# Optimization experiments

Hardware: AMD Instinct MI355X
Metric: run time of the kernel (lower is better)

## Reference

```python
import jax, jax.numpy as jnp
import numpy as np

B, N, NPOINT, NSAMPLE, CIN = 8, 16384, 2048, 32, 64
MLP = (64, 64, 128)
EPS = 1e-5  # torch BatchNorm2d default eps


def setup_inputs() -> dict:
    key = jax.random.key(0)
    ks = jax.random.split(key, 8)
    xyz = jax.random.normal(ks[0], (B, 3, N), dtype=jnp.float32)
    points = jax.random.normal(ks[1], (B, CIN, N), dtype=jnp.float32)
    # torch.randperm(N)[:npoint], shared across batch
    sample_idx = jax.random.permutation(ks[2], N)[:NPOINT].astype(jnp.int32)
    c0 = CIN + 3
    def conv_w(k, o, i):
        return jax.random.normal(k, (o, i), dtype=jnp.float32) * np.float32(1.0 / np.sqrt(i))
    W1 = conv_w(ks[3], MLP[0], c0)
    W2 = conv_w(ks[4], MLP[1], MLP[0])
    W3 = conv_w(ks[5], MLP[2], MLP[1])
    return {
        "xyz": xyz, "points": points, "sample_idx": sample_idx,
        "W1": W1, "b1": jnp.zeros((MLP[0],), jnp.float32), "g1": jnp.ones((MLP[0],), jnp.float32), "be1": jnp.zeros((MLP[0],), jnp.float32),
        "W2": W2, "b2": jnp.zeros((MLP[1],), jnp.float32), "g2": jnp.ones((MLP[1],), jnp.float32), "be2": jnp.zeros((MLP[1],), jnp.float32),
        "W3": W3, "b3": jnp.zeros((MLP[2],), jnp.float32), "g3": jnp.ones((MLP[2],), jnp.float32), "be3": jnp.zeros((MLP[2],), jnp.float32),
    }


def _bn(h, g, b):
    # training-mode BatchNorm2d: per-channel (last axis) stats over all other dims, biased var
    m = jnp.mean(h, axis=(0, 1, 2), keepdims=True)
    v = jnp.mean(jnp.square(h - m), axis=(0, 1, 2), keepdims=True)
    return (h - m) * jax.lax.rsqrt(v + EPS) * g + b


def reference(xyz, points, sample_idx, W1, b1, g1, be1, W2, b2, g2, be2, W3, b3, g3, be3):
    # sample npoint centroids (shared indices across batch, as in the torch code)
    q = jnp.take(xyz, sample_idx, axis=2).transpose(0, 2, 1)   # (B, npoint, 3)
    p = xyz.transpose(0, 2, 1)                                  # (B, N, 3)
    # squared pairwise distances (same ordering as cdist for topk)
    d2 = (jnp.sum(q * q, -1)[:, :, None]
          + jnp.sum(p * p, -1)[:, None, :]
          - 2.0 * jnp.einsum('bqc,bnc->bqn', q, p))             # (B, npoint, N)
    _, idx = jax.lax.top_k(-d2, NSAMPLE)                        # (B, npoint, nsample) smallest dists

    gxyz = jnp.take_along_axis(p[:, None, :, :], idx[:, :, :, None], axis=2)  # (B, npoint, nsample, 3)
    rel = gxyz - q[:, :, None, :]
    pf = points.transpose(0, 2, 1)                              # (B, N, C)
    gpts = jnp.take_along_axis(pf[:, None, :, :], idx[:, :, :, None], axis=2)  # (B, npoint, nsample, C)
    feat = jnp.concatenate([rel, gpts], axis=-1)                # (B, npoint, nsample, 3+C)

    h = jax.nn.relu(_bn(jnp.einsum('bpsc,oc->bpso', feat, W1) + b1, g1, be1))
    h = jax.nn.relu(_bn(jnp.einsum('bpsc,oc->bpso', h, W2) + b2, g2, be2))
    h = _bn(jnp.einsum('bpsc,oc->bpso', h, W3) + b3, g3, be3)
    new_points = jnp.max(h, axis=2)                             # max over nsample -> (B, npoint, mlp2)
    return q.transpose(0, 2, 1), new_points.transpose(0, 2, 1)  # (B,3,npoint), (B,mlp2,npoint)
```

## Files before the change

### kernel.cpp

```cpp
#include <hip/hip_runtime.h>
#include <cstdint>

#define DEVFN __device__ __forceinline__

constexpr int B_ = 8, N_ = 16384, NP_ = 2048, NS_ = 32;
constexpr int S_ = B_ * NP_ * NS_;
constexpr float INV_CNT = 1.0f / 524288.0f;

typedef __attribute__((ext_vector_type(8))) short bf8_t;
typedef __attribute__((ext_vector_type(4))) float f4_t;
#define MFMA16(A, Bv, C) __builtin_amdgcn_mfma_f32_16x16x32_bf16(A, Bv, C, 0, 0, 0)

union u4s8 { uint4 u; unsigned short s[8]; };

DEVFN unsigned long long wredmin64(unsigned long long v) {
  for (int o = 32; o; o >>= 1) { unsigned long long u = __shfl_xor(v, o); v = u < v ? u : v; }
  return v;
}
DEVFN float d2_ref(float4 q, float4 p) {
  float dot = __fadd_rn(__fadd_rn(__fmul_rn(q.x, p.x), __fmul_rn(q.y, p.y)), __fmul_rn(q.z, p.z));
  return __fsub_rn(__fadd_rn(q.w, p.w), __fadd_rn(dot, dot));
}
DEVFN unsigned int fmono(float d) {
  unsigned int u = __float_as_uint(d);
  return u ^ ((u >> 31) ? 0xFFFFFFFFu : 0x80000000u);
}
DEVFN unsigned short f2bf(float f) {
  unsigned int u = __float_as_uint(f);
  u += 0x7FFFu + ((u >> 16) & 1u);
  return (unsigned short)(u >> 16);
}
DEVFN bf8_t ld_bf8(const unsigned short* p) {
  union { uint4 u; bf8_t b; } cv;
  cv.u = *reinterpret_cast<const uint4*>(p);
  return cv.b;
}

__global__ __launch_bounds__(256) void prep_xyzw(const float* __restrict__ xyz, float4* __restrict__ xyzw) {
  int t = blockIdx.x * 256 + threadIdx.x;
  int b = t >> 14, n = t & (N_ - 1);
  const float* X = xyz + (size_t)b * 3 * N_;
  float x = X[n], y = X[N_ + n], z = X[2 * N_ + n];
  float sq = __fadd_rn(__fadd_rn(__fmul_rn(x, x), __fmul_rn(y, y)), __fmul_rn(z, z));
  xyzw[t] = make_float4(x, y, z, sq);
}

__global__ __launch_bounds__(256) void prep_q(const int* __restrict__ sidx, const float4* __restrict__ xyzw,
                                              float4* __restrict__ qw, float* __restrict__ out_q) {
  int t = blockIdx.x * 256 + threadIdx.x;
  int b = t >> 11, p = t & (NP_ - 1);
  int n = sidx[p] & (N_ - 1);
  float4 v = xyzw[b * N_ + n];
  qw[t] = v;
  out_q[((size_t)b * 3 + 0) * NP_ + p] = v.x;
  out_q[((size_t)b * 3 + 1) * NP_ + p] = v.y;
  out_q[((size_t)b * 3 + 2) * NP_ + p] = v.z;
}

__global__ __launch_bounds__(256) void transpose_bf16(const float* __restrict__ in, unsigned short* __restrict__ out) {
  __shared__ float tile[32][33];
  int b = blockIdx.x >> 10;
  int rem = blockIdx.x & 1023;
  int c0 = (rem >> 9) << 5;
  int n0 = (rem & 511) << 5;
  int tx = threadIdx.x & 31, ty = threadIdx.x >> 5;
#pragma unroll
  for (int jj = 0; jj < 4; jj++) {
    int c = c0 + ty + jj * 8;
    tile[ty + jj * 8][tx] = in[((size_t)b * 64 + c) * N_ + n0 + tx];
  }
  __syncthreads();
#pragma unroll
  for (int jj = 0; jj < 4; jj++) {
    int n = n0 + ty + jj * 8;
    out[((size_t)b * N_ + n) * 64 + c0 + tx] = f2bf(tile[tx][ty + jj * 8]);
  }
}

__global__ __launch_bounds__(256) void prep_w(const float* __restrict__ W1, const float* __restrict__ W2,
                                              const float* __restrict__ W3, unsigned short* __restrict__ W1b,
                                              unsigned short* __restrict__ W2b, unsigned short* __restrict__ W3b) {
  int t = blockIdx.x * 256 + threadIdx.x;
  int stride = gridDim.x * 256;
  for (int e = t; e < 64 * 96; e += stride) {
    int o = e / 96, k = e - o * 96;
    float v = (k < 64) ? W1[o * 67 + 3 + k] : (k < 67 ? W1[o * 67 + (k - 64)] : 0.0f);
    W1b[e] = f2bf(v);
  }
  for (int e = t; e < 64 * 64; e += stride) W2b[e] = f2bf(W2[e]);
  for (int e = t; e < 128 * 64; e += stride) W3b[e] = f2bf(W3[e]);
}

__global__ __launch_bounds__(256, 4) void knn_kernel(const float4* __restrict__ xyzw,
                                                     const float4* __restrict__ qw,
                                                     int* __restrict__ idx_out) {
  __shared__ float4 Pst[1024];
  __shared__ unsigned short surv[16][256];
  __shared__ float Tsh[16];
  __shared__ int cnt[16];
  int tid = threadIdx.x, wave = tid >> 6, lane = tid & 63;
  int b = blockIdx.x >> 7;
  int q0 = (blockIdx.x & 127) * 16;
  const float4* P = xyzw + b * N_;
  float Qx[16], Qy[16], Qz[16];
#pragma unroll
  for (int j = 0; j < 16; j++) {
    float4 q = qw[b * NP_ + q0 + j];
    Qx[j] = q.x; Qy[j] = q.y; Qz[j] = q.z;
  }
  float dmin[16];
#pragma unroll
  for (int j = 0; j < 16; j++) dmin[j] = 1e30f;
  for (int c = 0; c < N_ / 1024; c++) {
    __syncthreads();
#pragma unroll
    for (int u = 0; u < 4; u++) Pst[tid + u * 256] = P[c * 1024 + tid + u * 256];
    __syncthreads();
#pragma unroll
    for (int t = 0; t < 4; t++) {
      float4 p = Pst[wave * 256 + t * 64 + lane];
      float kx = -2.0f * p.x, ky = -2.0f * p.y, kz = -2.0f * p.z;
#pragma unroll
      for (int j = 0; j < 16; j++) {
        float key = __fmaf_rn(kx, Qx[j], __fmaf_rn(ky, Qy[j], __fmaf_rn(kz, Qz[j], p.w)));
        dmin[j] = fminf(dmin[j], key);
      }
    }
  }
  __syncthreads();
  float* dl = (float*)Pst;
#pragma unroll
  for (int j = 0; j < 16; j++) dl[j * 256 + wave * 64 + lane] = dmin[j];
  if (tid < 16) cnt[tid] = 0;
  __syncthreads();
#pragma unroll 1
  for (int jj = 0; jj < 4; jj++) {
    int j = wave * 4 + jj;
    float v = fminf(fminf(dl[j * 256 + lane], dl[j * 256 + 64 + lane]),
                    fminf(dl[j * 256 + 128 + lane], dl[j * 256 + 192 + lane]));
#pragma unroll
    for (int k = 2; k <= 64; k <<= 1)
#pragma unroll
      for (int s = k >> 1; s > 0; s >>= 1) {
        float o = __shfl_xor(v, s);
        bool up = ((lane & k) == 0);
        bool tmin = (((lane & s) == 0) == up);
        v = tmin ? fminf(v, o) : fmaxf(v, o);
      }
    if (lane == 31) Tsh[j] = v;
  }
  __syncthreads();
  float T[16];
#pragma unroll
  for (int j = 0; j < 16; j++) T[j] = Tsh[j];
  for (int c = 0; c < N_ / 1024; c++) {
    __syncthreads();
#pragma unroll
    for (int u = 0; u < 4; u++) Pst[tid + u * 256] = P[c * 1024 + tid + u * 256];
    __syncthreads();
#pragma unroll 1
    for (int t = 0; t < 4; t++) {
      int n = c * 1024 + wave * 256 + t * 64 + lane;
      float4 p = Pst[wave * 256 + t * 64 + lane];
      float kx = -2.0f * p.x, ky = -2.0f * p.y, kz = -2.0f * p.z;
#pragma unroll
      for (int j = 0; j < 16; j++) {
        float key = __fmaf_rn(kx, Qx[j], __fmaf_rn(ky, Qy[j], __fmaf_rn(kz, Qz[j], p.w)));
        bool pred = key <= T[j];
        unsigned long long mask = __ballot(pred);
        if (mask) {
          int basew;
          if (lane == 0) basew = atomicAdd(&cnt[j], (int)__popcll(mask));
          basew = __shfl(basew, 0);
          if (pred) {
            int off = basew + (int)__popcll(mask & ((1ull << lane) - 1ull));
            if (off < 256) surv[j][off] = (unsigned short)n;
          }
        }
      }
    }
  }
  __syncthreads();
#pragma unroll 1
  for (int jj = 0; jj < 4; jj++) {
    int j = wave * 4 + jj;
    float4 Q = qw[b * NP_ + q0 + j];
    int m = cnt[j] < 256 ? cnt[j] : 256;
    if (m <= 64) {
      unsigned long long v = ~0ull;
      if (lane < m) {
        int n = surv[j][lane];
        float4 p = P[n];
        float d2 = d2_ref(Q, p);
        v = ((unsigned long long)fmono(d2) << 32) | (unsigned int)n;
      }
#pragma unroll
      for (int k = 2; k <= 64; k <<= 1)
#pragma unroll
        for (int s = k >> 1; s > 0; s >>= 1) {
          unsigned long long o = __shfl_xor(v, s);
          bool up = ((lane & k) == 0);
          bool tmin = (((lane & s) == 0) == up);
          unsigned long long lo = v < o ? v : o;
          unsigned long long hi = v < o ? o : v;
          v = tmin ? lo : hi;
        }
      if (lane < 32) idx_out[(b * NP_ + q0 + j) * NS_ + lane] = (int)(v & 0xFFFFu);
    } else {
      unsigned long long k4[4];
#pragma unroll
      for (int t = 0; t < 4; t++) {
        int ii = t * 64 + lane;
        k4[t] = ~0ull;
        if (ii < m) {
          int n = surv[j][ii];
          float4 p = P[n];
          float d2 = d2_ref(Q, p);
          k4[t] = ((unsigned long long)fmono(d2) << 32) | (unsigned int)n;
        }
      }
      int keep = 0;
      for (int r = 0; r < 32; r++) {
        unsigned long long loc = k4[0];
        loc = k4[1] < loc ? k4[1] : loc;
        loc = k4[2] < loc ? k4[2] : loc;
        loc = k4[3] < loc ? k4[3] : loc;
        unsigned long long km = wredmin64(loc);
#pragma unroll
        for (int t = 0; t < 4; t++) if (k4[t] == km) k4[t] = ~0ull;
        if (lane == r) keep = (int)(km & 0xFFFFu);
      }
      if (lane < 32) idx_out[(b * NP_ + q0 + j) * NS_ + lane] = keep;
    }
  }
}


__global__ __launch_bounds__(256, 4) void fused1_mat(
    const int* __restrict__ idx, const float4* __restrict__ xyzw, const float4* __restrict__ qw,
    const unsigned short* __restrict__ pTb, const unsigned short* __restrict__ W1b,
    const float* __restrict__ b1, float* __restrict__ statsOut, unsigned short* __restrict__ h) {
  __shared__ unsigned short W1L[64 * 104];
  __shared__ unsigned short hbuf[64 * 64];
  __shared__ float sAcc[128];
  int tid = threadIdx.x;
  int w = tid >> 6, l = tid & 63;
  int c16 = l & 15, g = l >> 4;
  for (int e = tid; e < 64 * 12; e += 256) {
    int r = e / 12, c = e % 12;
    *(uint4*)&W1L[r * 104 + c * 8] = *(const uint4*)&W1b[r * 96 + c * 8];
  }
  float rb1[4];
#pragma unroll
  for (int j = 0; j < 4; j++) rb1[j] = b1[j * 16 + c16];
  float st1[4] = {0, 0, 0, 0}, st2[4] = {0, 0, 0, 0};
  __syncthreads();
  for (int tile = blockIdx.x; tile < S_ / 64; tile += gridDim.x) {
    int b = tile >> 10;
    int s = tile * 64 + w * 16 + c16;
    int n = idx[s] & (N_ - 1);
    const unsigned short* arow = pTb + (((size_t)(b << 14) + n) << 6);
    bf8_t a0 = ld_bf8(arow + g * 8);
    bf8_t a1 = ld_bf8(arow + 32 + g * 8);
    float4 P = xyzw[(b << 14) + n];
    float4 Q = qw[tile * 2 + (w >> 1)];
    bf8_t a2 = {0, 0, 0, 0, 0, 0, 0, 0};
    if (g == 0) {
      a2[0] = (short)f2bf(P.x - Q.x);
      a2[1] = (short)f2bf(P.y - Q.y);
      a2[2] = (short)f2bf(P.z - Q.z);
    }
    f4_t acc1[4];
#pragma unroll
    for (int j = 0; j < 4; j++) {
      bf8_t w0 = ld_bf8(&W1L[(j * 16 + c16) * 104 + 0 * 32 + g * 8]);
      bf8_t w1 = ld_bf8(&W1L[(j * 16 + c16) * 104 + 1 * 32 + g * 8]);
      bf8_t w2 = ld_bf8(&W1L[(j * 16 + c16) * 104 + 2 * 32 + g * 8]);
      acc1[j] = (f4_t){0.0f, 0.0f, 0.0f, 0.0f};
      acc1[j] = MFMA16(a0, w0, acc1[j]);
      acc1[j] = MFMA16(a1, w1, acc1[j]);
      acc1[j] = MFMA16(a2, w2, acc1[j]);
    }
    __syncthreads();
#pragma unroll
    for (int j = 0; j < 4; j++)
#pragma unroll
      for (int r = 0; r < 4; r++) {
        float hv = acc1[j][r] + rb1[j];
        st1[j] += hv; st2[j] += hv * hv;
        int row = w * 16 + g * 4 + r, ch = j * 16 + c16;
        hbuf[row * 64 + (((ch >> 3) ^ (row & 7)) << 3) + (ch & 7)] = f2bf(hv);
      }
    __syncthreads();
    int rrow = w * 16 + c16;
    uint4 v0 = *(const uint4*)&hbuf[rrow * 64 + ((g ^ (rrow & 7)) << 3)];
    uint4 v1 = *(const uint4*)&hbuf[rrow * 64 + (((4 + g) ^ (rrow & 7)) << 3)];
    uint4* hd = (uint4*)(h + (((size_t)tile * 64 + rrow) << 6));
    hd[g] = v0;
    hd[4 + g] = v1;
  }
  __syncthreads();
  if (tid < 128) sAcc[tid] = 0.0f;
  __syncthreads();
#pragma unroll
  for (int j = 0; j < 4; j++) {
    atomicAdd(&sAcc[j * 16 + c16], st1[j]);
    atomicAdd(&sAcc[64 + j * 16 + c16], st2[j]);
  }
  __syncthreads();
  if (tid < 128) atomicAdd(&statsOut[tid], sAcc[tid]);
}

__global__ __launch_bounds__(256, 4) void fused2_mat(
    const unsigned short* __restrict__ W2b, const float* __restrict__ g1, const float* __restrict__ be1,
    const float* __restrict__ stats1, const float* __restrict__ b2,
    float* __restrict__ statsOut, unsigned short* __restrict__ h) {
  __shared__ unsigned short W2L[64 * 72];
  __shared__ unsigned short hbuf[64 * 64];
  __shared__ float sa1[64], sd1[64];
  __shared__ float sAcc[128];
  int tid = threadIdx.x;
  int w = tid >> 6, l = tid & 63;
  int c16 = l & 15, g = l >> 4;
  for (int e = tid; e < 64 * 8; e += 256) {
    int r = e >> 3, c = e & 7;
    *(uint4*)&W2L[r * 72 + c * 8] = *(const uint4*)&W2b[r * 64 + c * 8];
  }
  if (tid < 64) {
    float m = stats1[tid] * INV_CNT;
    float v = stats1[64 + tid] * INV_CNT - m * m;
    float a = rsqrtf(v + 1e-5f) * g1[tid];
    sa1[tid] = a;
    sd1[tid] = be1[tid] - m * a;
  }
  float rb2[4];
#pragma unroll
  for (int j = 0; j < 4; j++) rb2[j] = b2[j * 16 + c16];
  float st1[4] = {0, 0, 0, 0}, st2[4] = {0, 0, 0, 0};
  __syncthreads();
  for (int tile = blockIdx.x; tile < S_ / 64; tile += gridDim.x) {
    int rrow = w * 16 + c16;
    uint4* hd = (uint4*)(h + (((size_t)tile * 64 + rrow) << 6));
    u4s8 c0, c1;
    c0.u = hd[g];
    c1.u = hd[4 + g];
    bf8_t a0f, a1f;
#pragma unroll
    for (int e = 0; e < 8; e++) {
      float x0 = __uint_as_float((unsigned)c0.s[e] << 16);
      float x1 = __uint_as_float((unsigned)c1.s[e] << 16);
      a0f[e] = (short)f2bf(fmaxf(0.0f, fmaf(x0, sa1[g * 8 + e], sd1[g * 8 + e])));
      a1f[e] = (short)f2bf(fmaxf(0.0f, fmaf(x1, sa1[32 + g * 8 + e], sd1[32 + g * 8 + e])));
    }
    f4_t acc2[4];
#pragma unroll
    for (int j = 0; j < 4; j++) {
      bf8_t w0 = ld_bf8(&W2L[(j * 16 + c16) * 72 + g * 8]);
      bf8_t w1 = ld_bf8(&W2L[(j * 16 + c16) * 72 + 32 + g * 8]);
      acc2[j] = (f4_t){0.0f, 0.0f, 0.0f, 0.0f};
      acc2[j] = MFMA16(a0f, w0, acc2[j]);
      acc2[j] = MFMA16(a1f, w1, acc2[j]);
    }
    __syncthreads();
#pragma unroll
    for (int j = 0; j < 4; j++)
#pragma unroll
      for (int r = 0; r < 4; r++) {
        float hv = acc2[j][r] + rb2[j];
        st1[j] += hv; st2[j] += hv * hv;
        int row = w * 16 + g * 4 + r, ch = j * 16 + c16;
        hbuf[row * 64 + (((ch >> 3) ^ (row & 7)) << 3) + (ch & 7)] = f2bf(hv);
      }
    __syncthreads();
    uint4 v0 = *(const uint4*)&hbuf[rrow * 64 + ((g ^ (rrow & 7)) << 3)];
    uint4 v1 = *(const uint4*)&hbuf[rrow * 64 + (((4 + g) ^ (rrow & 7)) << 3)];
    hd[g] = v0;
    hd[4 + g] = v1;
  }
  __syncthreads();
  if (tid < 128) sAcc[tid] = 0.0f;
  __syncthreads();
#pragma unroll
  for (int j = 0; j < 4; j++) {
    atomicAdd(&sAcc[j * 16 + c16], st1[j]);
    atomicAdd(&sAcc[64 + j * 16 + c16], st2[j]);
  }
  __syncthreads();
  if (tid < 128) atomicAdd(&statsOut[tid], sAcc[tid]);
}

__global__ __launch_bounds__(256, 4) void fused3_mat(
    const unsigned short* __restrict__ W3b, const float* __restrict__ g2, const float* __restrict__ be2,
    const float* __restrict__ stats2, const float* __restrict__ b3,
    float* __restrict__ statsOut, const unsigned short* __restrict__ h, float* __restrict__ maxmin) {
  __shared__ unsigned short W3L[128 * 72];
  __shared__ float sa2[64], sd2[64];
  __shared__ float smx[4][128];
  __shared__ float smn[4][128];
  __shared__ float sAcc[256];
  int tid = threadIdx.x;
  int w = tid >> 6, l = tid & 63;
  int c16 = l & 15, g = l >> 4;
  for (int e = tid; e < 128 * 8; e += 256) {
    int r = e >> 3, c = e & 7;
    *(uint4*)&W3L[r * 72 + c * 8] = *(const uint4*)&W3b[r * 64 + c * 8];
  }
  if (tid < 64) {
    float m = stats2[tid] * INV_CNT;
    float v = stats2[64 + tid] * INV_CNT - m * m;
    float a = rsqrtf(v + 1e-5f) * g2[tid];
    sa2[tid] = a;
    sd2[tid] = be2[tid] - m * a;
  }
  float rb3[8];
#pragma unroll
  for (int j = 0; j < 8; j++) rb3[j] = b3[j * 16 + c16];
  float st1[8], st2[8];
#pragma unroll
  for (int j = 0; j < 8; j++) { st1[j] = 0.0f; st2[j] = 0.0f; }
  __syncthreads();
  for (int tile = blockIdx.x; tile < S_ / 64; tile += gridDim.x) {
    int rrow = w * 16 + c16;
    const uint4* hd = (const uint4*)(h + (((size_t)tile * 64 + rrow) << 6));
    u4s8 c0, c1;
    c0.u = hd[g];
    c1.u = hd[4 + g];
    bf8_t a0f, a1f;
#pragma unroll
    for (int e = 0; e < 8; e++) {
      float x0 = __uint_as_float((unsigned)c0.s[e] << 16);
      float x1 = __uint_as_float((unsigned)c1.s[e] << 16);
      a0f[e] = (short)f2bf(fmaxf(0.0f, fmaf(x0, sa2[g * 8 + e], sd2[g * 8 + e])));
      a1f[e] = (short)f2bf(fmaxf(0.0f, fmaf(x1, sa2[32 + g * 8 + e], sd2[32 + g * 8 + e])));
    }
    f4_t acc3[8];
#pragma unroll
    for (int j = 0; j < 8; j++) {
      bf8_t w0 = ld_bf8(&W3L[(j * 16 + c16) * 72 + g * 8]);
      bf8_t w1 = ld_bf8(&W3L[(j * 16 + c16) * 72 + 32 + g * 8]);
      acc3[j] = (f4_t){0.0f, 0.0f, 0.0f, 0.0f};
      acc3[j] = MFMA16(a0f, w0, acc3[j]);
      acc3[j] = MFMA16(a1f, w1, acc3[j]);
    }
    float mx[8], mn[8];
#pragma unroll
    for (int j = 0; j < 8; j++) {
      mx[j] = -1e30f; mn[j] = 1e30f;
#pragma unroll
      for (int r = 0; r < 4; r++) {
        float hv = acc3[j][r] + rb3[j];
        st1[j] += hv; st2[j] += hv * hv;
        mx[j] = fmaxf(mx[j], hv); mn[j] = fminf(mn[j], hv);
      }
      mx[j] = fmaxf(mx[j], __shfl_xor(mx[j], 16));
      mx[j] = fmaxf(mx[j], __shfl_xor(mx[j], 32));
      mn[j] = fminf(mn[j], __shfl_xor(mn[j], 16));
      mn[j] = fminf(mn[j], __shfl_xor(mn[j], 32));
    }
    __syncthreads();
    if (l < 16) {
#pragma unroll
      for (int j = 0; j < 8; j++) { smx[w][j * 16 + l] = mx[j]; smn[w][j * 16 + l] = mn[j]; }
    }
    __syncthreads();
    {
      int cen = tid >> 7, ch = tid & 127;
      float vx = fmaxf(smx[2 * cen][ch], smx[2 * cen + 1][ch]);
      float vn = fminf(smn[2 * cen][ch], smn[2 * cen + 1][ch]);
      size_t gcen = (size_t)tile * 2 + cen;
      maxmin[gcen * 256 + ch * 2 + 0] = vx;
      maxmin[gcen * 256 + ch * 2 + 1] = vn;
    }
  }
  __syncthreads();
  if (tid < 256) sAcc[tid] = 0.0f;
  __syncthreads();
#pragma unroll
  for (int j = 0; j < 8; j++) {
    atomicAdd(&sAcc[j * 16 + c16], st1[j]);
    atomicAdd(&sAcc[128 + j * 16 + c16], st2[j]);
  }
  __syncthreads();
  if (tid < 256) atomicAdd(&statsOut[tid], sAcc[tid]);
}

template <int STAGES>
__global__ __launch_bounds__(256, (STAGES == 1) ? 4 : 3) void fused_kernel(
    const int* __restrict__ idx, const float4* __restrict__ xyzw, const float4* __restrict__ qw,
    const unsigned short* __restrict__ pTb, const unsigned short* __restrict__ W1b,
    const unsigned short* __restrict__ W2b, const unsigned short* __restrict__ W3b,
    const float* __restrict__ b1, const float* __restrict__ g1, const float* __restrict__ be1,
    const float* __restrict__ stats1,
    const float* __restrict__ b2, const float* __restrict__ g2, const float* __restrict__ be2,
    const float* __restrict__ stats2,
    const float* __restrict__ b3,
    float* __restrict__ statsOut, float* __restrict__ maxmin) {
  __shared__ unsigned short W1L[64 * 104];
  __shared__ unsigned short W2L[(STAGES >= 2) ? 64 * 72 : 8];
  __shared__ unsigned short W3L[(STAGES == 3) ? 128 * 72 : 8];
  __shared__ unsigned short hbuf[(STAGES >= 2) ? 64 * 64 : 8];
  __shared__ float smx[(STAGES == 3) ? 4 : 1][128];
  __shared__ float smn[(STAGES == 3) ? 4 : 1][128];
  __shared__ float sAcc[256];
  constexpr int NJL = (STAGES == 3) ? 8 : 4;
  int tid = threadIdx.x;
  int w = tid >> 6, l = tid & 63;
  int c16 = l & 15, g = l >> 4;
  for (int e = tid; e < 64 * 12; e += 256) {
    int r = e / 12, c = e % 12;
    *(uint4*)&W1L[r * 104 + c * 8] = *(const uint4*)&W1b[r * 96 + c * 8];
  }
  if (STAGES >= 2)
    for (int e = tid; e < 64 * 8; e += 256) {
      int r = e >> 3, c = e & 7;
      *(uint4*)&W2L[r * 72 + c * 8] = *(const uint4*)&W2b[r * 64 + c * 8];
    }
  if (STAGES == 3)
    for (int e = tid; e < 128 * 8; e += 256) {
      int r = e >> 3, c = e & 7;
      *(uint4*)&W3L[r * 72 + c * 8] = *(const uint4*)&W3b[r * 64 + c * 8];
    }
  float rb1[4], ra1[4], rd1[4], rb2[4], ra2[4], rd2[4], rb3[8];
#pragma unroll
  for (int j = 0; j < 4; j++) rb1[j] = b1[j * 16 + c16];
  if (STAGES >= 2) {
#pragma unroll
    for (int j = 0; j < 4; j++) {
      int ch = j * 16 + c16;
      float m = stats1[ch] * INV_CNT;
      float v = stats1[64 + ch] * INV_CNT - m * m;
      float a = rsqrtf(v + 1e-5f) * g1[ch];
      ra1[j] = a; rd1[j] = be1[ch] - m * a;
      rb2[j] = b2[ch];
    }
  }
  if (STAGES == 3) {
#pragma unroll
    for (int j = 0; j < 4; j++) {
      int ch = j * 16 + c16;
      float m = stats2[ch] * INV_CNT;
      float v = stats2[64 + ch] * INV_CNT - m * m;
      float a = rsqrtf(v + 1e-5f) * g2[ch];
      ra2[j] = a; rd2[j] = be2[ch] - m * a;
    }
#pragma unroll
    for (int j = 0; j < 8; j++) rb3[j] = b3[j * 16 + c16];
  }
  float st1[NJL], st2[NJL];
#pragma unroll
  for (int j = 0; j < NJL; j++) { st1[j] = 0.0f; st2[j] = 0.0f; }
  __syncthreads();
  for (int tile = blockIdx.x; tile < S_ / 64; tile += gridDim.x) {
    int b = tile >> 10;
    int s = tile * 64 + w * 16 + c16;
    int n = idx[s] & (N_ - 1);
    const unsigned short* arow = pTb + (((size_t)(b << 14) + n) << 6);
    bf8_t a0 = ld_bf8(arow + g * 8);
    bf8_t a1 = ld_bf8(arow + 32 + g * 8);
    float4 P = xyzw[(b << 14) + n];
    float4 Q = qw[tile * 2 + (w >> 1)];
    bf8_t a2 = {0, 0, 0, 0, 0, 0, 0, 0};
    if (g == 0) {
      a2[0] = (short)f2bf(P.x - Q.x);
      a2[1] = (short)f2bf(P.y - Q.y);
      a2[2] = (short)f2bf(P.z - Q.z);
    }
    f4_t acc1[4];
#pragma unroll
    for (int j = 0; j < 4; j++) {
      bf8_t w0 = ld_bf8(&W1L[(j * 16 + c16) * 104 + 0 * 32 + g * 8]);
      bf8_t w1 = ld_bf8(&W1L[(j * 16 + c16) * 104 + 1 * 32 + g * 8]);
      bf8_t w2 = ld_bf8(&W1L[(j * 16 + c16) * 104 + 2 * 32 + g * 8]);
      acc1[j] = (f4_t){0.0f, 0.0f, 0.0f, 0.0f};
      acc1[j] = MFMA16(a0, w0, acc1[j]);
      acc1[j] = MFMA16(a1, w1, acc1[j]);
      acc1[j] = MFMA16(a2, w2, acc1[j]);
    }
    if (STAGES == 1) {
#pragma unroll
      for (int j = 0; j < 4; j++)
#pragma unroll
        for (int r = 0; r < 4; r++) {
          float hv = acc1[j][r] + rb1[j];
          st1[j] += hv; st2[j] += hv * hv;
        }
      continue;
    }
    if (STAGES == 2) __syncthreads();
#pragma unroll
    for (int j = 0; j < 4; j++)
#pragma unroll
      for (int r = 0; r < 4; r++) {
        float hv = acc1[j][r] + rb1[j];
        float t = fmaxf(0.0f, fmaf(hv, ra1[j], rd1[j]));
        int row = w * 16 + g * 4 + r, ch = j * 16 + c16;
        hbuf[row * 64 + (((ch >> 3) ^ (row & 7)) << 3) + (ch & 7)] = f2bf(t);
      }
    __syncthreads();
    int rrow = w * 16 + c16;
    bf8_t h1f[2];
#pragma unroll
    for (int kb = 0; kb < 2; kb++)
      h1f[kb] = ld_bf8(hbuf + rrow * 64 + (((kb * 4 + g) ^ (rrow & 7)) << 3));
    f4_t acc2[4];
#pragma unroll
    for (int j = 0; j < 4; j++) {
      bf8_t w0 = ld_bf8(&W2L[(j * 16 + c16) * 72 + g * 8]);
      bf8_t w1 = ld_bf8(&W2L[(j * 16 + c16) * 72 + 32 + g * 8]);
      acc2[j] = (f4_t){0.0f, 0.0f, 0.0f, 0.0f};
      acc2[j] = MFMA16(h1f[0], w0, acc2[j]);
      acc2[j] = MFMA16(h1f[1], w1, acc2[j]);
    }
    if (STAGES == 2) {
#pragma unroll
      for (int j = 0; j < 4; j++)
#pragma unroll
        for (int r = 0; r < 4; r++) {
          float hv = acc2[j][r] + rb2[j];
          st1[j] += hv; st2[j] += hv * hv;
        }
      continue;
    }
    __syncthreads();
#pragma unroll
    for (int j = 0; j < 4; j++)
#pragma unroll
      for (int r = 0; r < 4; r++) {
        float hv = acc2[j][r] + rb2[j];
        float t = fmaxf(0.0f, fmaf(hv, ra2[j], rd2[j]));
        int row = w * 16 + g * 4 + r, ch = j * 16 + c16;
        hbuf[row * 64 + (((ch >> 3) ^ (row & 7)) << 3) + (ch & 7)] = f2bf(t);
      }
    __syncthreads();
    bf8_t h2f[2];
#pragma unroll
    for (int kb = 0; kb < 2; kb++)
      h2f[kb] = ld_bf8(hbuf + rrow * 64 + (((kb * 4 + g) ^ (rrow & 7)) << 3));
    f4_t acc3[8];
#pragma unroll
    for (int j = 0; j < 8; j++) {
      bf8_t w0 = ld_bf8(&W3L[(j * 16 + c16) * 72 + g * 8]);
      bf8_t w1 = ld_bf8(&W3L[(j * 16 + c16) * 72 + 32 + g * 8]);
      acc3[j] = (f4_t){0.0f, 0.0f, 0.0f, 0.0f};
      acc3[j] = MFMA16(h2f[0], w0, acc3[j]);
      acc3[j] = MFMA16(h2f[1], w1, acc3[j]);
    }
    float mx[8], mn[8];
#pragma unroll
    for (int j = 0; j < 8; j++) {
      mx[j] = -1e30f; mn[j] = 1e30f;
#pragma unroll
      for (int r = 0; r < 4; r++) {
        float hv = acc3[j][r] + rb3[j];
        st1[j] += hv; st2[j] += hv * hv;
        mx[j] = fmaxf(mx[j], hv); mn[j] = fminf(mn[j], hv);
      }
      mx[j] = fmaxf(mx[j], __shfl_xor(mx[j], 16));
      mx[j] = fmaxf(mx[j], __shfl_xor(mx[j], 32));
      mn[j] = fminf(mn[j], __shfl_xor(mn[j], 16));
      mn[j] = fminf(mn[j], __shfl_xor(mn[j], 32));
    }
    if (l < 16) {
#pragma unroll
      for (int j = 0; j < 8; j++) { smx[w][j * 16 + l] = mx[j]; smn[w][j * 16 + l] = mn[j]; }
    }
    __syncthreads();
    {
      int cen = tid >> 7, ch = tid & 127;
      float vx = fmaxf(smx[2 * cen][ch], smx[2 * cen + 1][ch]);
      float vn = fminf(smn[2 * cen][ch], smn[2 * cen + 1][ch]);
      size_t gcen = (size_t)tile * 2 + cen;
      maxmin[gcen * 256 + ch * 2 + 0] = vx;
      maxmin[gcen * 256 + ch * 2 + 1] = vn;
    }
  }
  __syncthreads();
  if (tid < 2 * NJL * 16) sAcc[tid] = 0.0f;
  __syncthreads();
#pragma unroll
  for (int j = 0; j < NJL; j++) {
    atomicAdd(&sAcc[j * 16 + c16], st1[j]);
    atomicAdd(&sAcc[NJL * 16 + j * 16 + c16], st2[j]);
  }
  __syncthreads();
  if (tid < 2 * NJL * 16) atomicAdd(&statsOut[tid], sAcc[tid]);
}

__global__ __launch_bounds__(256) void finalize_kernel(const float* __restrict__ maxmin,
                                                       const float* __restrict__ stats3,
                                                       const float* __restrict__ g3, const float* __restrict__ be3,
                                                       float* __restrict__ out_np) {
  int o = blockIdx.x * 256 + threadIdx.x;
  int p = o & 2047, ch = (o >> 11) & 127, b = o >> 18;
  float m = stats3[ch] * INV_CNT;
  float v = stats3[128 + ch] * INV_CNT - m * m;
  float a = rsqrtf(v + 1e-5f) * g3[ch];
  float d = be3[ch] - m * a;
  size_t g = (size_t)(b * 2048 + p);
  float hi = maxmin[g * 256 + ch * 2 + 0];
  float lo = maxmin[g * 256 + ch * 2 + 1];
  out_np[o] = fmaf(a, (a >= 0.0f ? hi : lo), d);
}

extern "C" void kernel_launch(void* const* d_in, const int* in_sizes, int n_in,
                              void* d_out, int out_size, void* d_ws, size_t ws_size,
                              hipStream_t stream) {
  const float* xyz = (const float*)d_in[0];
  const float* points = (const float*)d_in[1];
  const int* sidx = (const int*)d_in[2];
  const float* W1 = (const float*)d_in[3];
  const float* b1 = (const float*)d_in[4];
  const float* g1 = (const float*)d_in[5];
  const float* be1 = (const float*)d_in[6];
  const float* W2 = (const float*)d_in[7];
  const float* b2 = (const float*)d_in[8];
  const float* g2 = (const float*)d_in[9];
  const float* be2 = (const float*)d_in[10];
  const float* W3 = (const float*)d_in[11];
  const float* b3 = (const float*)d_in[12];
  const float* g3 = (const float*)d_in[13];
  const float* be3 = (const float*)d_in[14];

  float* out_q = (float*)d_out;
  float* out_np = (float*)d_out + (size_t)B_ * 3 * NP_;

  char* ws = (char*)d_ws;
  float* stats1 = (float*)(ws + 0);
  float* stats2 = (float*)(ws + 512);
  float* stats3 = (float*)(ws + 1024);
  size_t off = 4096;
  float4* xyzw = (float4*)(ws + off); off += (size_t)B_ * N_ * 16;
  float4* qw = (float4*)(ws + off);   off += (size_t)B_ * NP_ * 16;
  int* idxb = (int*)(ws + off);       off += (size_t)B_ * NP_ * NS_ * 4;
  unsigned short* pTb = (unsigned short*)(ws + off); off += (size_t)B_ * N_ * 64 * 2;
  unsigned short* W1b = (unsigned short*)(ws + off); off += 64 * 96 * 2;
  unsigned short* W2b = (unsigned short*)(ws + off); off += 64 * 64 * 2;
  unsigned short* W3b = (unsigned short*)(ws + off); off += 128 * 64 * 2;
  float* maxmin = (float*)(ws + off);  off += (size_t)B_ * NP_ * 128 * 2 * 4;
  unsigned short* hG = (unsigned short*)(ws + off); off += (size_t)S_ * 64 * 2;
  bool use_mat = (ws_size >= off);

  hipMemsetAsync(ws, 0, 4096, stream);
  prep_xyzw<<<B_ * N_ / 256, 256, 0, stream>>>(xyz, xyzw);
  prep_q<<<B_ * NP_ / 256, 256, 0, stream>>>(sidx, xyzw, qw, out_q);
  transpose_bf16<<<B_ * 2 * (N_ / 32), 256, 0, stream>>>(points, pTb);
  prep_w<<<72, 256, 0, stream>>>(W1, W2, W3, W1b, W2b, W3b);
  knn_kernel<<<B_ * (NP_ / 16), 256, 0, stream>>>(xyzw, qw, idxb);
  if (use_mat) {
    fused1_mat<<<1024, 256, 0, stream>>>(idxb, xyzw, qw, pTb, W1b, b1, stats1, hG);
    fused2_mat<<<1024, 256, 0, stream>>>(W2b, g1, be1, stats1, b2, stats2, hG);
    fused3_mat<<<1024, 256, 0, stream>>>(W3b, g2, be2, stats2, b3, stats3, hG, maxmin);
  } else {
    fused_kernel<1><<<1024, 256, 0, stream>>>(idxb, xyzw, qw, pTb, W1b, W2b, W3b,
        b1, g1, be1, stats1, b2, g2, be2, stats2, b3, stats1, maxmin);
    fused_kernel<2><<<1024, 256, 0, stream>>>(idxb, xyzw, qw, pTb, W1b, W2b, W3b,
        b1, g1, be1, stats1, b2, g2, be2, stats2, b3, stats2, maxmin);
    fused_kernel<3><<<1024, 256, 0, stream>>>(idxb, xyzw, qw, pTb, W1b, W2b, W3b,
        b1, g1, be1, stats1, b2, g2, be2, stats2, b3, stats3, maxmin);
  }
  finalize_kernel<<<(B_ * 128 * NP_) / 256, 256, 0, stream>>>(maxmin, stats3, g3, be3, out_np);
}
```

Measured before the change: 403.6 us.

## Give each wave its own centroid to drop block-wide barriers in MLP stages

The three materialized MLP kernels now assign one centroid (32 samples) to each wave instead of a 64-row tile shared by the block. Each wave gets a private LDS staging buffer, and the block __syncthreads calls become wave barriers. Stage 3 reduces max/min within the wave and writes it directly as float2, with no shared-memory cross-wave merge. The grid doubles to 2048 blocks, and the fallback recompute path and the workspace-size check are removed, so the code now assumes the workspace is large enough.

```diff
diff --git a/kernel.cpp b/kernel.cpp
--- a/kernel.cpp
+++ b/kernel.cpp
@@ -241,7 +241,7 @@
     const unsigned short* __restrict__ pTb, const unsigned short* __restrict__ W1b,
     const float* __restrict__ b1, float* __restrict__ statsOut, unsigned short* __restrict__ h) {
   __shared__ unsigned short W1L[64 * 104];
-  __shared__ unsigned short hbuf[64 * 64];
+  __shared__ unsigned short hb[4][32 * 64];
   __shared__ float sAcc[128];
   int tid = threadIdx.x;
   int w = tid >> 6, l = tid & 63;
@@ -255,49 +255,56 @@
   for (int j = 0; j < 4; j++) rb1[j] = b1[j * 16 + c16];
   float st1[4] = {0, 0, 0, 0}, st2[4] = {0, 0, 0, 0};
   __syncthreads();
-  for (int tile = blockIdx.x; tile < S_ / 64; tile += gridDim.x) {
-    int b = tile >> 10;
-    int s = tile * 64 + w * 16 + c16;
-    int n = idx[s] & (N_ - 1);
-    const unsigned short* arow = pTb + (((size_t)(b << 14) + n) << 6);
-    bf8_t a0 = ld_bf8(arow + g * 8);
-    bf8_t a1 = ld_bf8(arow + 32 + g * 8);
-    float4 P = xyzw[(b << 14) + n];
-    float4 Q = qw[tile * 2 + (w >> 1)];
-    bf8_t a2 = {0, 0, 0, 0, 0, 0, 0, 0};
-    if (g == 0) {
-      a2[0] = (short)f2bf(P.x - Q.x);
-      a2[1] = (short)f2bf(P.y - Q.y);
-      a2[2] = (short)f2bf(P.z - Q.z);
-    }
-    f4_t acc1[4];
-#pragma unroll
-    for (int j = 0; j < 4; j++) {
-      bf8_t w0 = ld_bf8(&W1L[(j * 16 + c16) * 104 + 0 * 32 + g * 8]);
-      bf8_t w1 = ld_bf8(&W1L[(j * 16 + c16) * 104 + 1 * 32 + g * 8]);
-      bf8_t w2 = ld_bf8(&W1L[(j * 16 + c16) * 104 + 2 * 32 + g * 8]);
-      acc1[j] = (f4_t){0.0f, 0.0f, 0.0f, 0.0f};
-      acc1[j] = MFMA16(a0, w0, acc1[j]);
-      acc1[j] = MFMA16(a1, w1, acc1[j]);
-      acc1[j] = MFMA16(a2, w2, acc1[j]);
-    }
-    __syncthreads();
-#pragma unroll
-    for (int j = 0; j < 4; j++)
-#pragma unroll
-      for (int r = 0; r < 4; r++) {
-        float hv = acc1[j][r] + rb1[j];
-        st1[j] += hv; st2[j] += hv * hv;
-        int row = w * 16 + g * 4 + r, ch = j * 16 + c16;
-        hbuf[row * 64 + (((ch >> 3) ^ (row & 7)) << 3) + (ch & 7)] = f2bf(hv);
-      }
-    __syncthreads();
-    int rrow = w * 16 + c16;
-    uint4 v0 = *(const uint4*)&hbuf[rrow * 64 + ((g ^ (rrow & 7)) << 3)];
-    uint4 v1 = *(const uint4*)&hbuf[rrow * 64 + (((4 + g) ^ (rrow & 7)) << 3)];
-    uint4* hd = (uint4*)(h + (((size_t)tile * 64 + rrow) << 6));
-    hd[g] = v0;
-    hd[4 + g] = v1;
+  unsigned short* hw = hb[w];
+  for (int cen = blockIdx.x * 4 + w; cen < B_ * NP_; cen += gridDim.x * 4) {
+    int b = cen >> 11;
+    float4 Q = qw[cen];
+#pragma unroll
+    for (int rh = 0; rh < 2; rh++) {
+      int s = cen * 32 + rh * 16 + c16;
+      int n = idx[s] & (N_ - 1);
+      const unsigned short* arow = pTb + (((size_t)(b << 14) + n) << 6);
+      bf8_t a0 = ld_bf8(arow + g * 8);
+      bf8_t a1 = ld_bf8(arow + 32 + g * 8);
+      float4 P = xyzw[(b << 14) + n];
+      bf8_t a2 = {0, 0, 0, 0, 0, 0, 0, 0};
+      if (g == 0) {
+        a2[0] = (short)f2bf(P.x - Q.x);
+        a2[1] = (short)f2bf(P.y - Q.y);
+        a2[2] = (short)f2bf(P.z - Q.z);
+      }
+      f4_t acc[4];
+#pragma unroll
+      for (int j = 0; j < 4; j++) {
+        bf8_t w0 = ld_bf8(&W1L[(j * 16 + c16) * 104 + 0 * 32 + g * 8]);
+        bf8_t w1 = ld_bf8(&W1L[(j * 16 + c16) * 104 + 1 * 32 + g * 8]);
+        bf8_t w2 = ld_bf8(&W1L[(j * 16 + c16) * 104 + 2 * 32 + g * 8]);
+        acc[j] = (f4_t){0.0f, 0.0f, 0.0f, 0.0f};
+        acc[j] = MFMA16(a0, w0, acc[j]);
+        acc[j] = MFMA16(a1, w1, acc[j]);
+        acc[j] = MFMA16(a2, w2, acc[j]);
+      }
+#pragma unroll
+      for (int j = 0; j < 4; j++)
+#pragma unroll
+        for (int r = 0; r < 4; r++) {
+          float hv = acc[j][r] + rb1[j];
+          st1[j] += hv; st2[j] += hv * hv;
+          int row = rh * 16 + g * 4 + r, ch = j * 16 + c16;
+          hw[row * 64 + (((ch >> 3) ^ (row & 7)) << 3) + (ch & 7)] = f2bf(hv);
+        }
+    }
+    __builtin_amdgcn_wave_barrier();
+#pragma unroll
+    for (int rh = 0; rh < 2; rh++) {
+      int rr = rh * 16 + c16;
+      uint4 v0 = *(const uint4*)&hw[rr * 64 + ((g ^ (rr & 7)) << 3)];
+      uint4 v1 = *(const uint4*)&hw[rr * 64 + (((4 + g) ^ (rr & 7)) << 3)];
+      uint4* hd = (uint4*)(h + (((size_t)cen * 32 + rr) << 6));
+      hd[g] = v0;
+      hd[4 + g] = v1;
+    }
+    __builtin_amdgcn_wave_barrier();
   }
   __syncthreads();
   if (tid < 128) sAcc[tid] = 0.0f;
@@ -316,7 +323,7 @@
     const float* __restrict__ stats1, const float* __restrict__ b2,
     float* __restrict__ statsOut, unsigned short* __restrict__ h) {
   __shared__ unsigned short W2L[64 * 72];
-  __shared__ unsigned short hbuf[64 * 64];
+  __shared__ unsigned short hb[4][32 * 64];
   __shared__ float sa1[64], sd1[64];
   __shared__ float sAcc[128];
   int tid = threadIdx.x;
@@ -338,44 +345,53 @@
   for (int j = 0; j < 4; j++) rb2[j] = b2[j * 16 + c16];
   float st1[4] = {0, 0, 0, 0}, st2[4] = {0, 0, 0, 0};
   __syncthreads();
-  for (int tile = blockIdx.x; tile < S_ / 64; tile += gridDim.x) {
-    int rrow = w * 16 + c16;
-    uint4* hd = (uint4*)(h + (((size_t)tile * 64 + rrow) << 6));
-    u4s8 c0, c1;
-    c0.u = hd[g];
-    c1.u = hd[4 + g];
-    bf8_t a0f, a1f;
-#pragma unroll
-    for (int e = 0; e < 8; e++) {
-      float x0 = __uint_as_float((unsigned)c0.s[e] << 16);
-      float x1 = __uint_as_float((unsigned)c1.s[e] << 16);
-      a0f[e] = (short)f2bf(fmaxf(0.0f, fmaf(x0, sa1[g * 8 + e], sd1[g * 8 + e])));
-      a1f[e] = (short)f2bf(fmaxf(0.0f, fmaf(x1, sa1[32 + g * 8 + e], sd1[32 + g * 8 + e])));
-    }
-    f4_t acc2[4];
-#pragma unroll
-    for (int j = 0; j < 4; j++) {
-      bf8_t w0 = ld_bf8(&W2L[(j * 16 + c16) * 72 + g * 8]);
-      bf8_t w1 = ld_bf8(&W2L[(j * 16 + c16) * 72 + 32 + g * 8]);
-      acc2[j] = (f4_t){0.0f, 0.0f, 0.0f, 0.0f};
-      acc2[j] = MFMA16(a0f, w0, acc2[j]);
-      acc2[j] = MFMA16(a1f, w1, acc2[j]);
-    }
-    __syncthreads();
-#pragma unroll
-    for (int j = 0; j < 4; j++)
-#pragma unroll
-      for (int r = 0; r < 4; r++) {
-        float hv = acc2[j][r] + rb2[j];
-        st1[j] += hv; st2[j] += hv * hv;
-        int row = w * 16 + g * 4 + r, ch = j * 16 + c16;
-        hbuf[row * 64 + (((ch >> 3) ^ (row & 7)) << 3) + (ch & 7)] = f2bf(hv);
-      }
-    __syncthreads();
-    uint4 v0 = *(const uint4*)&hbuf[rrow * 64 + ((g ^ (rrow & 7)) << 3)];
-    uint4 v1 = *(const uint4*)&hbuf[rrow * 64 + (((4 + g) ^ (rrow & 7)) << 3)];
-    hd[g] = v0;
-    hd[4 + g] = v1;
+  unsigned short* hw = hb[w];
+  for (int cen = blockIdx.x * 4 + w; cen < B_ * NP_; cen += gridDim.x * 4) {
+#pragma unroll
+    for (int rh = 0; rh < 2; rh++) {
+      int rr = rh * 16 + c16;
+      uint4* hd = (uint4*)(h + (((size_t)cen * 32 + rr) << 6));
+      u4s8 c0, c1;
+      c0.u = hd[g];
+      c1.u = hd[4 + g];
+      bf8_t a0f, a1f;
+#pragma unroll
+      for (int e = 0; e < 8; e++) {
+        float x0 = __uint_as_float((unsigned)c0.s[e] << 16);
+        float x1 = __uint_as_float((unsigned)c1.s[e] << 16);
+        a0f[e] = (short)f2bf(fmaxf(0.0f, fmaf(x0, sa1[g * 8 + e], sd1[g * 8 + e])));
+        a1f[e] = (short)f2bf(fmaxf(0.0f, fmaf(x1, sa1[32 + g * 8 + e], sd1[32 + g * 8 + e])));
+      }
+      f4_t acc[4];
+#pragma unroll
+      for (int j = 0; j < 4; j++) {
+        bf8_t w0 = ld_bf8(&W2L[(j * 16 + c16) * 72 + g * 8]);
+        bf8_t w1 = ld_bf8(&W2L[(j * 16 + c16) * 72 + 32 + g * 8]);
+        acc[j] = (f4_t){0.0f, 0.0f, 0.0f, 0.0f};
+        acc[j] = MFMA16(a0f, w0, acc[j]);
+        acc[j] = MFMA16(a1f, w1, acc[j]);
+      }
+#pragma unroll
+      for (int j = 0; j < 4; j++)
+#pragma unroll
+        for (int r = 0; r < 4; r++) {
+          float hv = acc[j][r] + rb2[j];
+          st1[j] += hv; st2[j] += hv * hv;
+          int row = rh * 16 + g * 4 + r, ch = j * 16 + c16;
+          hw[row * 64 + (((ch >> 3) ^ (row & 7)) << 3) + (ch & 7)] = f2bf(hv);
+        }
+    }
+    __builtin_amdgcn_wave_barrier();
+#pragma unroll
+    for (int rh = 0; rh < 2; rh++) {
+      int rr = rh * 16 + c16;
+      uint4 v0 = *(const uint4*)&hw[rr * 64 + ((g ^ (rr & 7)) << 3)];
+      uint4 v1 = *(const uint4*)&hw[rr * 64 + (((4 + g) ^ (rr & 7)) << 3)];
+      uint4* hd = (uint4*)(h + (((size_t)cen * 32 + rr) << 6));
+      hd[g] = v0;
+      hd[4 + g] = v1;
+    }
+    __builtin_amdgcn_wave_barrier();
   }
   __syncthreads();
   if (tid < 128) sAcc[tid] = 0.0f;
@@ -395,8 +411,6 @@
     float* __restrict__ statsOut, const unsigned short* __restrict__ h, float* __restrict__ maxmin) {
   __shared__ unsigned short W3L[128 * 72];
   __shared__ float sa2[64], sd2[64];
-  __shared__ float smx[4][128];
-  __shared__ float smn[4][128];
   __shared__ float sAcc[256];
   int tid = threadIdx.x;
   int w = tid >> 6, l = tid & 63;
@@ -419,57 +433,54 @@
 #pragma unroll
   for (int j = 0; j < 8; j++) { st1[j] = 0.0f; st2[j] = 0.0f; }
   __syncthreads();
-  for (int tile = blockIdx.x; tile < S_ / 64; tile += gridDim.x) {
-    int rrow = w * 16 + c16;
-    const uint4* hd = (const uint4*)(h + (((size_t)tile * 64 + rrow) << 6));
-    u4s8 c0, c1;
-    c0.u = hd[g];
-    c1.u = hd[4 + g];
-    bf8_t a0f, a1f;
-#pragma unroll
-    for (int e = 0; e < 8; e++) {
-      float x0 = __uint_as_float((unsigned)c0.s[e] << 16);
-      float x1 = __uint_as_float((unsigned)c1.s[e] << 16);
-      a0f[e] = (short)f2bf(fmaxf(0.0f, fmaf(x0, sa2[g * 8 + e], sd2[g * 8 + e])));
-      a1f[e] = (short)f2bf(fmaxf(0.0f, fmaf(x1, sa2[32 + g * 8 + e], sd2[32 + g * 8 + e])));
-    }
-    f4_t acc3[8];
+  for (int cen = blockIdx.x * 4 + w; cen < B_ * NP_; cen += gridDim.x * 4) {
+    float mx[8], mn[8];
+#pragma unroll
+    for (int j = 0; j < 8; j++) { mx[j] = -1e30f; mn[j] = 1e30f; }
+#pragma unroll
+    for (int rh = 0; rh < 2; rh++) {
+      int rr = rh * 16 + c16;
+      const uint4* hd = (const uint4*)(h + (((size_t)cen * 32 + rr) << 6));
+      u4s8 c0, c1;
+      c0.u = hd[g];
+      c1.u = hd[4 + g];
+      bf8_t a0f, a1f;
+#pragma unroll
+      for (int e = 0; e < 8; e++) {
+        float x0 = __uint_as_float((unsigned)c0.s[e] << 16);
+        float x1 = __uint_as_float((unsigned)c1.s[e] << 16);
+        a0f[e] = (short)f2bf(fmaxf(0.0f, fmaf(x0, sa2[g * 8 + e], sd2[g * 8 + e])));
+        a1f[e] = (short)f2bf(fmaxf(0.0f, fmaf(x1, sa2[32 + g * 8 + e], sd2[32 + g * 8 + e])));
+      }
+      f4_t acc[8];
+#pragma unroll
+      for (int j = 0; j < 8; j++) {
+        bf8_t w0 = ld_bf8(&W3L[(j * 16 + c16) * 72 + g * 8]);
+        bf8_t w1 = ld_bf8(&W3L[(j * 16 + c16) * 72 + 32 + g * 8]);
+        acc[j] = (f4_t){0.0f, 0.0f, 0.0f, 0.0f};
+        acc[j] = MFMA16(a0f, w0, acc[j]);
+        acc[j] = MFMA16(a1f, w1, acc[j]);
+      }
+#pragma unroll
+      for (int j = 0; j < 8; j++)
+#pragma unroll
+        for (int r = 0; r < 4; r++) {
+          float hv = acc[j][r] + rb3[j];
+          st1[j] += hv; st2[j] += hv * hv;
+          mx[j] = fmaxf(mx[j], hv); mn[j] = fminf(mn[j], hv);
+        }
+    }
 #pragma unroll
     for (int j = 0; j < 8; j++) {
-      bf8_t w0 = ld_bf8(&W3L[(j * 16 + c16) * 72 + g * 8]);
-      bf8_t w1 = ld_bf8(&W3L[(j * 16 + c16) * 72 + 32 + g * 8]);
-      acc3[j] = (f4_t){0.0f, 0.0f, 0.0f, 0.0f};
-      acc3[j] = MFMA16(a0f, w0, acc3[j]);
-      acc3[j] = MFMA16(a1f, w1, acc3[j]);
-    }
-    float mx[8], mn[8];
-#pragma unroll
-    for (int j = 0; j < 8; j++) {
-      mx[j] = -1e30f; mn[j] = 1e30f;
-#pragma unroll
-      for (int r = 0; r < 4; r++) {
-        float hv = acc3[j][r] + rb3[j];
-        st1[j] += hv; st2[j] += hv * hv;
-        mx[j] = fmaxf(mx[j], hv); mn[j] = fminf(mn[j], hv);
-      }
       mx[j] = fmaxf(mx[j], __shfl_xor(mx[j], 16));
       mx[j] = fmaxf(mx[j], __shfl_xor(mx[j], 32));
       mn[j] = fminf(mn[j], __shfl_xor(mn[j], 16));
       mn[j] = fminf(mn[j], __shfl_xor(mn[j], 32));
     }
-    __syncthreads();
     if (l < 16) {
-#pragma unroll
-      for (int j = 0; j < 8; j++) { smx[w][j * 16 + l] = mx[j]; smn[w][j * 16 + l] = mn[j]; }
-    }
-    __syncthreads();
-    {
-      int cen = tid >> 7, ch = tid & 127;
-      float vx = fmaxf(smx[2 * cen][ch], smx[2 * cen + 1][ch]);
-      float vn = fminf(smn[2 * cen][ch], smn[2 * cen + 1][ch]);
-      size_t gcen = (size_t)tile * 2 + cen;
-      maxmin[gcen * 256 + ch * 2 + 0] = vx;
-      maxmin[gcen * 256 + ch * 2 + 1] = vn;
+      float2* mm = (float2*)(maxmin + (size_t)cen * 256);
+#pragma unroll
+      for (int j = 0; j < 8; j++) mm[j * 16 + l] = make_float2(mx[j], mn[j]);
     }
   }
   __syncthreads();
@@ -482,208 +493,6 @@
   }
   __syncthreads();
   if (tid < 256) atomicAdd(&statsOut[tid], sAcc[tid]);
-}
-
-template <int STAGES>
-__global__ __launch_bounds__(256, (STAGES == 1) ? 4 : 3) void fused_kernel(
-    const int* __restrict__ idx, const float4* __restrict__ xyzw, const float4* __restrict__ qw,
-    const unsigned short* __restrict__ pTb, const unsigned short* __restrict__ W1b,
-    const unsigned short* __restrict__ W2b, const unsigned short* __restrict__ W3b,
-    const float* __restrict__ b1, const float* __restrict__ g1, const float* __restrict__ be1,
-    const float* __restrict__ stats1,
-    const float* __restrict__ b2, const float* __restrict__ g2, const float* __restrict__ be2,
-    const float* __restrict__ stats2,
-    const float* __restrict__ b3,
-    float* __restrict__ statsOut, float* __restrict__ maxmin) {
-  __shared__ unsigned short W1L[64 * 104];
-  __shared__ unsigned short W2L[(STAGES >= 2) ? 64 * 72 : 8];
-  __shared__ unsigned short W3L[(STAGES == 3) ? 128 * 72 : 8];
-  __shared__ unsigned short hbuf[(STAGES >= 2) ? 64 * 64 : 8];
-  __shared__ float smx[(STAGES == 3) ? 4 : 1][128];
-  __shared__ float smn[(STAGES == 3) ? 4 : 1][128];
-  __shared__ float sAcc[256];
-  constexpr int NJL = (STAGES == 3) ? 8 : 4;
-  int tid = threadIdx.x;
-  int w = tid >> 6, l = tid & 63;
-  int c16 = l & 15, g = l >> 4;
-  for (int e = tid; e < 64 * 12; e += 256) {
-    int r = e / 12, c = e % 12;
-    *(uint4*)&W1L[r * 104 + c * 8] = *(const uint4*)&W1b[r * 96 + c * 8];
-  }
-  if (STAGES >= 2)
-    for (int e = tid; e < 64 * 8; e += 256) {
-      int r = e >> 3, c = e & 7;
-      *(uint4*)&W2L[r * 72 + c * 8] = *(const uint4*)&W2b[r * 64 + c * 8];
-    }
-  if (STAGES == 3)
-    for (int e = tid; e < 128 * 8; e += 256) {
-      int r = e >> 3, c = e & 7;
-      *(uint4*)&W3L[r * 72 + c * 8] = *(const uint4*)&W3b[r * 64 + c * 8];
-    }
-  float rb1[4], ra1[4], rd1[4], rb2[4], ra2[4], rd2[4], rb3[8];
-#pragma unroll
-  for (int j = 0; j < 4; j++) rb1[j] = b1[j * 16 + c16];
-  if (STAGES >= 2) {
-#pragma unroll
-    for (int j = 0; j < 4; j++) {
-      int ch = j * 16 + c16;
-      float m = stats1[ch] * INV_CNT;
-      float v = stats1[64 + ch] * INV_CNT - m * m;
-      float a = rsqrtf(v + 1e-5f) * g1[ch];
-      ra1[j] = a; rd1[j] = be1[ch] - m * a;
-      rb2[j] = b2[ch];
-    }
-  }
-  if (STAGES == 3) {
-#pragma unroll
-    for (int j = 0; j < 4; j++) {
-      int ch = j * 16 + c16;
-      float m = stats2[ch] * INV_CNT;
-      float v = stats2[64 + ch] * INV_CNT - m * m;
-      float a = rsqrtf(v + 1e-5f) * g2[ch];
-      ra2[j] = a; rd2[j] = be2[ch] - m * a;
-    }
-#pragma unroll
-    for (int j = 0; j < 8; j++) rb3[j] = b3[j * 16 + c16];
-  }
-  float st1[NJL], st2[NJL];
-#pragma unroll
-  for (int j = 0; j < NJL; j++) { st1[j] = 0.0f; st2[j] = 0.0f; }
-  __syncthreads();
-  for (int tile = blockIdx.x; tile < S_ / 64; tile += gridDim.x) {
-    int b = tile >> 10;
-    int s = tile * 64 + w * 16 + c16;
-    int n = idx[s] & (N_ - 1);
-    const unsigned short* arow = pTb + (((size_t)(b << 14) + n) << 6);
-    bf8_t a0 = ld_bf8(arow + g * 8);
-    bf8_t a1 = ld_bf8(arow + 32 + g * 8);
-    float4 P = xyzw[(b << 14) + n];
-    float4 Q = qw[tile * 2 + (w >> 1)];
-    bf8_t a2 = {0, 0, 0, 0, 0, 0, 0, 0};
-    if (g == 0) {
-      a2[0] = (short)f2bf(P.x - Q.x);
-      a2[1] = (short)f2bf(P.y - Q.y);
-      a2[2] = (short)f2bf(P.z - Q.z);
-    }
-    f4_t acc1[4];
-#pragma unroll
-    for (int j = 0; j < 4; j++) {
-      bf8_t w0 = ld_bf8(&W1L[(j * 16 + c16) * 104 + 0 * 32 + g * 8]);
-      bf8_t w1 = ld_bf8(&W1L[(j * 16 + c16) * 104 + 1 * 32 + g * 8]);
-      bf8_t w2 = ld_bf8(&W1L[(j * 16 + c16) * 104 + 2 * 32 + g * 8]);
-      acc1[j] = (f4_t){0.0f, 0.0f, 0.0f, 0.0f};
-      acc1[j] = MFMA16(a0, w0, acc1[j]);
-      acc1[j] = MFMA16(a1, w1, acc1[j]);
-      acc1[j] = MFMA16(a2, w2, acc1[j]);
-    }
-    if (STAGES == 1) {
-#pragma unroll
-      for (int j = 0; j < 4; j++)
-#pragma unroll
-        for (int r = 0; r < 4; r++) {
-          float hv = acc1[j][r] + rb1[j];
-          st1[j] += hv; st2[j] += hv * hv;
-        }
-      continue;
-    }
-    if (STAGES == 2) __syncthreads();
-#pragma unroll
-    for (int j = 0; j < 4; j++)
-#pragma unroll
-      for (int r = 0; r < 4; r++) {
-        float hv = acc1[j][r] + rb1[j];
-        float t = fmaxf(0.0f, fmaf(hv, ra1[j], rd1[j]));
-        int row = w * 16 + g * 4 + r, ch = j * 16 + c16;
-        hbuf[row * 64 + (((ch >> 3) ^ (row & 7)) << 3) + (ch & 7)] = f2bf(t);
-      }
-    __syncthreads();
-    int rrow = w * 16 + c16;
-    bf8_t h1f[2];
-#pragma unroll
-    for (int kb = 0; kb < 2; kb++)
-      h1f[kb] = ld_bf8(hbuf + rrow * 64 + (((kb * 4 + g) ^ (rrow & 7)) << 3));
-    f4_t acc2[4];
-#pragma unroll
-    for (int j = 0; j < 4; j++) {
-      bf8_t w0 = ld_bf8(&W2L[(j * 16 + c16) * 72 + g * 8]);
-      bf8_t w1 = ld_bf8(&W2L[(j * 16 + c16) * 72 + 32 + g * 8]);
-      acc2[j] = (f4_t){0.0f, 0.0f, 0.0f, 0.0f};
-      acc2[j] = MFMA16(h1f[0], w0, acc2[j]);
-      acc2[j] = MFMA16(h1f[1], w1, acc2[j]);
-    }
-    if (STAGES == 2) {
-#pragma unroll
-      for (int j = 0; j < 4; j++)
-#pragma unroll
-        for (int r = 0; r < 4; r++) {
-          float hv = acc2[j][r] + rb2[j];
-          st1[j] += hv; st2[j] += hv * hv;
-        }
-      continue;
-    }
-    __syncthreads();
-#pragma unroll
-    for (int j = 0; j < 4; j++)
-#pragma unroll
-      for (int r = 0; r < 4; r++) {
-        float hv = acc2[j][r] + rb2[j];
-        float t = fmaxf(0.0f, fmaf(hv, ra2[j], rd2[j]));
-        int row = w * 16 + g * 4 + r, ch = j * 16 + c16;
-        hbuf[row * 64 + (((ch >> 3) ^ (row & 7)) << 3) + (ch & 7)] = f2bf(t);
-      }
-    __syncthreads();
-    bf8_t h2f[2];
-#pragma unroll
-    for (int kb = 0; kb < 2; kb++)
-      h2f[kb] = ld_bf8(hbuf + rrow * 64 + (((kb * 4 + g) ^ (rrow & 7)) << 3));
-    f4_t acc3[8];
-#pragma unroll
-    for (int j = 0; j < 8; j++) {
-      bf8_t w0 = ld_bf8(&W3L[(j * 16 + c16) * 72 + g * 8]);
-      bf8_t w1 = ld_bf8(&W3L[(j * 16 + c16) * 72 + 32 + g * 8]);
-      acc3[j] = (f4_t){0.0f, 0.0f, 0.0f, 0.0f};
-      acc3[j] = MFMA16(h2f[0], w0, acc3[j]);
-      acc3[j] = MFMA16(h2f[1], w1, acc3[j]);
-    }
-    float mx[8], mn[8];
-#pragma unroll
-    for (int j = 0; j < 8; j++) {
-      mx[j] = -1e30f; mn[j] = 1e30f;
-#pragma unroll
-      for (int r = 0; r < 4; r++) {
-        float hv = acc3[j][r] + rb3[j];
-        st1[j] += hv; st2[j] += hv * hv;
-        mx[j] = fmaxf(mx[j], hv); mn[j] = fminf(mn[j], hv);
-      }
-      mx[j] = fmaxf(mx[j], __shfl_xor(mx[j], 16));
-      mx[j] = fmaxf(mx[j], __shfl_xor(mx[j], 32));
-      mn[j] = fminf(mn[j], __shfl_xor(mn[j], 16));
-      mn[j] = fminf(mn[j], __shfl_xor(mn[j], 32));
-    }
-    if (l < 16) {
-#pragma unroll
-      for (int j = 0; j < 8; j++) { smx[w][j * 16 + l] = mx[j]; smn[w][j * 16 + l] = mn[j]; }
-    }
-    __syncthreads();
-    {
-      int cen = tid >> 7, ch = tid & 127;
-      float vx = fmaxf(smx[2 * cen][ch], smx[2 * cen + 1][ch]);
-      float vn = fminf(smn[2 * cen][ch], smn[2 * cen + 1][ch]);
-      size_t gcen = (size_t)tile * 2 + cen;
-      maxmin[gcen * 256 + ch * 2 + 0] = vx;
-      maxmin[gcen * 256 + ch * 2 + 1] = vn;
-    }
-  }
-  __syncthreads();
-  if (tid < 2 * NJL * 16) sAcc[tid] = 0.0f;
-  __syncthreads();
-#pragma unroll
-  for (int j = 0; j < NJL; j++) {
-    atomicAdd(&sAcc[j * 16 + c16], st1[j]);
-    atomicAdd(&sAcc[NJL * 16 + j * 16 + c16], st2[j]);
-  }
-  __syncthreads();
-  if (tid < 2 * NJL * 16) atomicAdd(&statsOut[tid], sAcc[tid]);
 }
 
 __global__ __launch_bounds__(256) void finalize_kernel(const float* __restrict__ maxmin,
@@ -738,7 +547,6 @@
   unsigned short* W3b = (unsigned short*)(ws + off); off += 128 * 64 * 2;
   float* maxmin = (float*)(ws + off);  off += (size_t)B_ * NP_ * 128 * 2 * 4;
   unsigned short* hG = (unsigned short*)(ws + off); off += (size_t)S_ * 64 * 2;
-  bool use_mat = (ws_size >= off);
 
   hipMemsetAsync(ws, 0, 4096, stream);
   prep_xyzw<<<B_ * N_ / 256, 256, 0, stream>>>(xyz, xyzw);
@@ -746,17 +554,8 @@
   transpose_bf16<<<B_ * 2 * (N_ / 32), 256, 0, stream>>>(points, pTb);
   prep_w<<<72, 256, 0, stream>>>(W1, W2, W3, W1b, W2b, W3b);
   knn_kernel<<<B_ * (NP_ / 16), 256, 0, stream>>>(xyzw, qw, idxb);
-  if (use_mat) {
-    fused1_mat<<<1024, 256, 0, stream>>>(idxb, xyzw, qw, pTb, W1b, b1, stats1, hG);
-    fused2_mat<<<1024, 256, 0, stream>>>(W2b, g1, be1, stats1, b2, stats2, hG);
-    fused3_mat<<<1024, 256, 0, stream>>>(W3b, g2, be2, stats2, b3, stats3, hG, maxmin);
-  } else {
-    fused_kernel<1><<<1024, 256, 0, stream>>>(idxb, xyzw, qw, pTb, W1b, W2b, W3b,
-        b1, g1, be1, stats1, b2, g2, be2, stats2, b3, stats1, maxmin);
-    fused_kernel<2><<<1024, 256, 0, stream>>>(idxb, xyzw, qw, pTb, W1b, W2b, W3b,
-        b1, g1, be1, stats1, b2, g2, be2, stats2, b3, stats2, maxmin);
-    fused_kernel<3><<<1024, 256, 0, stream>>>(idxb, xyzw, qw, pTb, W1b, W2b, W3b,
-        b1, g1, be1, stats1, b2, g2, be2, stats2, b3, stats3, maxmin);
-  }
+  fused1_mat<<<2048, 256, 0, stream>>>(idxb, xyzw, qw, pTb, W1b, b1, stats1, hG);
+  fused2_mat<<<2048, 256, 0, stream>>>(W2b, g1, be1, stats1, b2, stats2, hG);
+  fused3_mat<<<2048, 256, 0, stream>>>(W3b, g2, be2, stats2, b3, stats3, hG, maxmin);
   finalize_kernel<<<(B_ * 128 * NP_) / 256, 256, 0, stream>>>(maxmin, stats3, g3, be3, out_np);
 }
```

Result: slower. 598.2 us (+48.2%).
